# Kernel tuning notes

Measured on AMD Instinct MI355X. Metric: run time of the kernel, lower is better.

## Reference

```python
import jax, jax.numpy as jnp
import numpy as np

B, DIM, X, Y = 2, 256, 48, 48
HEADS, DIM_HEAD = 8, 64
DIM_INNER = HEADS * DIM_HEAD
MASK_SELF_VALUE = -100.0
EPS = 1e-12


def setup_inputs() -> dict:
    key = jax.random.key(0)
    k0, k1, k2, k3, k4 = jax.random.split(key, 5)
    return {
        "fmap": jax.random.normal(k0, (B, DIM, X, Y), dtype=jnp.float32),
        "gamma": jnp.ones((DIM,), dtype=jnp.float32),
        "w_qk": jax.random.normal(k1, (DIM_INNER, DIM), dtype=jnp.float32) * 0.02,
        "w_v": jax.random.normal(k2, (DIM_INNER, DIM), dtype=jnp.float32) * 0.02,
        "null_kv": jax.random.normal(k3, (2, HEADS, DIM_HEAD), dtype=jnp.float32),
        "w_out": jax.random.normal(k4, (DIM, DIM_INNER), dtype=jnp.float32) * 0.02,
    }


def _safe_sqrt(d2):
    # matches torch.cdist subgradient: zero grad at zero distance
    pos = d2 > 0
    return jnp.where(pos, jnp.sqrt(jnp.where(pos, d2, 1.0)), 0.0)


def reference(fmap, gamma, w_qk, w_v, null_kv, w_out):
    b, c, x, y = fmap.shape
    h, dh = HEADS, DIM_HEAD
    n = x * y
    scale = dh ** -0.5

    # ChannelRMSNorm: L2-normalize over channel dim, * sqrt(dim) * gamma
    l2 = jnp.sqrt(jnp.sum(fmap * fmap, axis=1, keepdims=True))
    normed = fmap / jnp.maximum(l2, EPS) * jnp.sqrt(jnp.float32(c)) * gamma[None, :, None, None]

    flat = normed.reshape(b, c, n)                       # b c n
    qk = jnp.einsum('oc,bcn->bon', w_qk, flat)           # b (h d) n
    v = jnp.einsum('oc,bcn->bon', w_v, flat)
    qk = qk.reshape(b, h, dh, n).transpose(0, 1, 3, 2)   # b h n d
    v = v.reshape(b, h, dh, n).transpose(0, 1, 3, 2)

    nk = jnp.broadcast_to(null_kv[0][None, :, None, :], (b, h, 1, dh))
    nv = jnp.broadcast_to(null_kv[1][None, :, None, :], (b, h, 1, dh))
    q = qk
    k = jnp.concatenate([nk, qk], axis=2)                # b h (n+1) d
    vv = jnp.concatenate([nv, v], axis=2)

    # -cdist(q, k, p=2) * scale via squared-distance expansion
    q2 = jnp.sum(q * q, axis=-1)[..., :, None]           # b h n 1
    k2 = jnp.sum(k * k, axis=-1)[..., None, :]           # b h 1 n+1
    cross = jnp.einsum('bhid,bhjd->bhij', q, k)          # b h n n+1
    d2 = jnp.maximum(q2 + k2 - 2.0 * cross, 0.0)
    sim = -_safe_sqrt(d2) * scale

    # mask self: eye(n) left-padded by one (null token never masked)
    self_mask = jnp.eye(n, n + 1, k=1, dtype=bool)
    sim = jnp.where(self_mask, MASK_SELF_VALUE, sim)

    attn = jax.nn.softmax(sim, axis=-1)
    out = jnp.einsum('bhij,bhjd->bhid', attn, vv)        # b h n d
    out = out.transpose(0, 1, 3, 2).reshape(b, h * dh, x, y)
    return jnp.einsum('oc,bcxy->boxy', w_out, out)
```

## Files before the change

kernel.cpp:

```cpp
#include <hip/hip_runtime.h>
#include <math.h>

#define NPOS 2304
#define CC   256
#define DI   512
#define NT   36
#define SCALE 0.125f
#define MASKV -100.0f
#define NEGSL2E (-0.18033688011112042f)

typedef __attribute__((ext_vector_type(8))) short bf16x8;
typedef __attribute__((ext_vector_type(4))) float f32x4;
typedef unsigned short u16;
typedef unsigned int u32;

__device__ inline u16 f2bf(float f) {
    union { float f; unsigned int u; } v; v.f = f;
    return (u16)((v.u + 0x7fffu + ((v.u >> 16) & 1u)) >> 16);
}
__device__ inline float bf2f(u16 h) { return __uint_as_float(((u32)h) << 16); }

__device__ inline bf16x8 ld_x8(const u16* p) {
    union { bf16x8 v; uint2 d[2]; } u;
    u.d[0] = *(const uint2*)(p + 0);
    u.d[1] = *(const uint2*)(p + 4);
    return u.v;
}

__device__ __forceinline__ void gl16(const u16* g, u16* l) {
    __builtin_amdgcn_global_load_lds(
        (const __attribute__((address_space(1))) void*)g,
        (__attribute__((address_space(3))) void*)l, 16, 0, 0);
}

__global__ __launch_bounds__(256) void k_pre(const float* __restrict__ fmap,
                                             const float* __restrict__ gamma,
                                             const float* __restrict__ wqk,
                                             const float* __restrict__ wv,
                                             const float* __restrict__ wout,
                                             u16* __restrict__ xn,
                                             u16* __restrict__ wqkh,
                                             u16* __restrict__ wvh,
                                             u16* __restrict__ wo_hi,
                                             u16* __restrict__ wo_lo) {
    const int blk = blockIdx.x;
    const int t = threadIdx.x;
    if (blk >= 72) {
        const int idx = blk - 72;
        if (idx < 128) {
            const int k = idx * 256 + t;
            const float4 v = ((const float4*)wqk)[k];
            ushort4 h4;
            h4.x = f2bf(v.x); h4.y = f2bf(v.y); h4.z = f2bf(v.z); h4.w = f2bf(v.w);
            ((ushort4*)wqkh)[k] = h4;
        } else if (idx < 256) {
            const int k = (idx - 128) * 256 + t;
            const float4 v = ((const float4*)wv)[k];
            ushort4 h4;
            h4.x = f2bf(v.x); h4.y = f2bf(v.y); h4.z = f2bf(v.z); h4.w = f2bf(v.w);
            ((ushort4*)wvh)[k] = h4;
        } else {
            const int k = (idx - 256) * 256 + t;
            const float4 v = ((const float4*)wout)[k];
            ushort4 h4, l4;
            h4.x = f2bf(v.x); l4.x = f2bf(v.x - bf2f(h4.x));
            h4.y = f2bf(v.y); l4.y = f2bf(v.y - bf2f(h4.y));
            h4.z = f2bf(v.z); l4.z = f2bf(v.z - bf2f(h4.z));
            h4.w = f2bf(v.w); l4.w = f2bf(v.w - bf2f(h4.w));
            ((ushort4*)wo_hi)[k] = h4;
            ((ushort4*)wo_lo)[k] = l4;
        }
        return;
    }
    const int b = blk & 1, n0 = (blk >> 1) * 64;
    const int tx = t & 63, ty = t >> 6;
    __shared__ u16 X[64][260];
    __shared__ float red[4][64];
    __shared__ float inv_s[64];
    __shared__ float gs[256];

    gs[t] = gamma[t];
    const float* fb = fmap + (size_t)b * CC * NPOS;
    float v64[64];
#pragma unroll
    for (int i = 0; i < 64; ++i)
        v64[i] = fb[(ty * 64 + i) * NPOS + n0 + tx];
    float s = 0.0f;
#pragma unroll
    for (int i = 0; i < 64; ++i) s += v64[i] * v64[i];
    red[ty][tx] = s;
    __syncthreads();
    if (t < 64) {
        const float tt = red[0][t] + red[1][t] + red[2][t] + red[3][t];
        inv_s[t] = 16.0f / fmaxf(sqrtf(tt), 1e-12f);
    }
    __syncthreads();
    const float iv = inv_s[tx];
#pragma unroll
    for (int i = 0; i < 64; i += 2) {
        const int c = ty * 64 + i;
        const float v0 = v64[i] * iv * gs[c];
        const float v1 = v64[i + 1] * iv * gs[c + 1];
        *(u32*)&X[tx][c] = (u32)f2bf(v0) | ((u32)f2bf(v1) << 16);
    }
    __syncthreads();
    u16* xb = xn + ((size_t)b * NPOS + n0) * 256;
#pragma unroll
    for (int k = 0; k < 8; ++k) {
        const int gran = k * 256 + t;
        const int row = gran >> 5, colg = gran & 31;
        const uint2 lo = *(const uint2*)&X[row][colg * 8];
        const uint2 hi = *(const uint2*)&X[row][colg * 8 + 4];
        *(uint4*)&xb[(size_t)gran * 8] = make_uint4(lo.x, lo.y, hi.x, hi.y);
    }
}

__global__ __launch_bounds__(256) void k_proj(const u16* __restrict__ xn,
                                              const u16* __restrict__ wqkh,
                                              const u16* __restrict__ wvh,
                                              const float* __restrict__ null_kv,
                                              u16* __restrict__ qkh,
                                              u16* __restrict__ vt,
                                              float* __restrict__ sq,
                                              float* __restrict__ ndot,
                                              float* __restrict__ nk2b) {
    const int blk = blockIdx.x;
    const int xcd = blk & 7;
    const int r   = blk >> 3;
    const int bh  = xcd * 2 + (r & 1);
    const int b   = bh >> 3;
    const int oy  = bh & 7;
    const int n0  = (r >> 1) * 64;

    const int t  = threadIdx.x;
    const int w = t >> 6, lane = t & 63, mcol = lane & 15, quad = lane >> 4;

    __shared__ __align__(16) u16 Xl[16384];
    __shared__ float sqp[4][64], ndp[4][64];
    u16 (*Tt)[68] = (u16(*)[68])Xl;

    const u16* xg = xn + ((size_t)b * NPOS + n0) * 256;
    {
        const int r01 = lane >> 5;
        const int jg = lane & 31;
#pragma unroll
        for (int rr = 0; rr < 8; ++rr) {
            const int row = rr * 8 + w * 2 + r01;
            gl16(xg + (size_t)row * 256 + (size_t)((jg ^ (row & 7)) * 8),
                 Xl + (rr * 8 + w * 2) * 256);
        }
    }
    if (blk == 0 && t < 8) {
        float s2 = 0.0f;
#pragma unroll 8
        for (int d = 0; d < 64; ++d) { const float x = null_kv[t * 64 + d]; s2 += x * x; }
        nk2b[t] = s2;
    }
    __syncthreads();

    const size_t wroff = (size_t)(oy * 64 + w * 16 + mcol) * 256 + quad * 8;
    const u16* wrq = wqkh + wroff;
    const u16* wrv = wvh + wroff;

    f32x4 cq[4], cv[4];
#pragma unroll
    for (int nf = 0; nf < 4; ++nf) {
        cq[nf] = (f32x4){0.f, 0.f, 0.f, 0.f};
        cv[nf] = (f32x4){0.f, 0.f, 0.f, 0.f};
    }
#pragma unroll
    for (int kc = 0; kc < 8; ++kc) {
        const bf16x8 aq = *(const bf16x8*)&wrq[kc * 32];
        const bf16x8 av = *(const bf16x8*)&wrv[kc * 32];
        bf16x8 xB[4];
#pragma unroll
        for (int nf = 0; nf < 4; ++nf) {
            const int row = nf * 16 + mcol;
            const int g = (kc * 4 + quad) ^ (row & 7);
            xB[nf] = *(const bf16x8*)&Xl[row * 256 + g * 8];
        }
#pragma unroll
        for (int nf = 0; nf < 4; ++nf) {
            cq[nf] = __builtin_amdgcn_mfma_f32_16x16x32_bf16(aq, xB[nf], cq[nf], 0, 0, 0);
            cv[nf] = __builtin_amdgcn_mfma_f32_16x16x32_bf16(av, xB[nf], cv[nf], 0, 0, 0);
        }
    }
    __syncthreads();

    {
        const int h = oy;
        const float4 nk4 = *(const float4*)&null_kv[h * 64 + w * 16 + quad * 4];
        float sv[4], nd[4];
#pragma unroll
        for (int nf = 0; nf < 4; ++nf) {
            sv[nf] = cq[nf][0] * cq[nf][0] + cq[nf][1] * cq[nf][1] + cq[nf][2] * cq[nf][2] + cq[nf][3] * cq[nf][3];
            nd[nf] = cq[nf][0] * nk4.x + cq[nf][1] * nk4.y + cq[nf][2] * nk4.z + cq[nf][3] * nk4.w;
        }
#pragma unroll
        for (int mk = 16; mk <= 32; mk <<= 1)
#pragma unroll
            for (int nf = 0; nf < 4; ++nf) {
                sv[nf] += __shfl_xor(sv[nf], mk);
                nd[nf] += __shfl_xor(nd[nf], mk);
            }
        if (quad == 0) {
#pragma unroll
            for (int nf = 0; nf < 4; ++nf) {
                sqp[w][nf * 16 + mcol] = sv[nf];
                ndp[w][nf * 16 + mcol] = nd[nf];
            }
        }
#pragma unroll
        for (int nf = 0; nf < 4; ++nf) {
            ushort4 r4;
            r4.x = f2bf(cq[nf][0]); r4.y = f2bf(cq[nf][1]);
            r4.z = f2bf(cq[nf][2]); r4.w = f2bf(cq[nf][3]);
            *(ushort4*)&Tt[nf * 16 + mcol][w * 16 + quad * 4] = r4;
        }
        __syncthreads();
        {
            const int n = t >> 2, ds = (t & 3) * 16;
            const uint2 r0 = *(const uint2*)&Tt[n][ds + 0];
            const uint2 r1 = *(const uint2*)&Tt[n][ds + 4];
            const uint2 r2 = *(const uint2*)&Tt[n][ds + 8];
            const uint2 r3 = *(const uint2*)&Tt[n][ds + 12];
            u16* dst = qkh + (((size_t)bh) * NPOS + n0 + n) * 64 + ds;
            *(uint4*)&dst[0] = make_uint4(r0.x, r0.y, r1.x, r1.y);
            *(uint4*)&dst[8] = make_uint4(r2.x, r2.y, r3.x, r3.y);
        }
        if (t < 64) {
            sq  [((size_t)bh) * NPOS + n0 + t] = sqp[0][t] + sqp[1][t] + sqp[2][t] + sqp[3][t];
            ndot[((size_t)bh) * NPOS + n0 + t] = ndp[0][t] + ndp[1][t] + ndp[2][t] + ndp[3][t];
        }
    }
    __syncthreads();

    {
#pragma unroll
        for (int nf = 0; nf < 4; ++nf)
#pragma unroll
            for (int rr = 0; rr < 4; ++rr)
                Tt[w * 16 + quad * 4 + rr][nf * 16 + mcol] = f2bf(cv[nf][rr]);
        __syncthreads();
        {
            const int d = t >> 2, ks = t & 3;
            const uint2 a0 = *(const uint2*)&Tt[d][ks * 16 + 0];
            const uint2 a1 = *(const uint2*)&Tt[d][ks * 16 + 4];
            const uint2 a2 = *(const uint2*)&Tt[d][ks * 16 + 8];
            const uint2 a3 = *(const uint2*)&Tt[d][ks * 16 + 12];
            u16* vdst = vt + (size_t)bh * (72 * 64 * 32);
            const int kb = (n0 >> 5) + (ks >> 1);
            u16* p = &vdst[((size_t)kb * 64 + d) * 32 + (ks & 1) * 16];
            *(uint4*)&p[0] = make_uint4(a0.x, a0.y, a1.x, a1.y);
            *(uint4*)&p[8] = make_uint4(a2.x, a2.y, a3.x, a3.y);
        }
    }
}

template <int KS>
__global__ __launch_bounds__(256) void k_attn(const u16* __restrict__ qkh,
                                              const u16* __restrict__ vt,
                                              const float* __restrict__ null_kv,
                                              const float* __restrict__ nk2b,
                                              const float* __restrict__ sq,
                                              const float* __restrict__ ndot,
                                              u16* __restrict__ ih,
                                              u16* __restrict__ il,
                                              float* __restrict__ pO,
                                              float* __restrict__ pL) {
    const int blk = blockIdx.x;
    const int xcd = blk & 7;
    const int j = blk >> 3;
    const int bh = xcd * 2 + (j & 1);
    const int r2 = j >> 1;
    const int qt = (KS == 2) ? (r2 >> 1) : r2;
    const int kh = (KS == 2) ? (r2 & 1) : 0;
    const int q0 = qt * 64;
    const int b = bh >> 3, h = bh & 7;
    const int t = threadIdx.x;
    const int wave = t >> 6, lane = t & 63;
    const int mcol = lane & 15, quad = lane >> 4;

    const int kt0 = kh * 18;
    const int NTL = (KS == 2) ? 18 : 36;

    __shared__ __align__(16) u16 sm[20480];
    u16* Kls = sm;
    u16* Vls = sm + 8192;
    u16 (*Pt)[64] = (u16(*)[64])(sm + 16384 + wave * 1024);

    const u16* qbase = qkh + (size_t)bh * NPOS * 64;
    const u16* vbase = vt + (size_t)bh * (72 * 64 * 32);
    const float* sqb = sq + (size_t)bh * NPOS;

    const int q16 = q0 + wave * 16;
    const bf16x8 bq00 = *(const bf16x8*)&qbase[(q16 + mcol) * 64 + quad * 8];
    const bf16x8 bq01 = *(const bf16x8*)&qbase[(q16 + mcol) * 64 + 32 + quad * 8];
    const float q2 = sqb[q16 + mcol];
    const int ktm = q16 >> 6;
    const int nbm = (q16 >> 4) & 3;

    const int kbase0 = (wave * 16 + 0) * 64;
    const int kbase1 = (wave * 16 + 8) * 64;
    const int ksrc0 = (wave * 16 + 0 + (lane >> 3)) * 64 + ((lane & 7) ^ (lane >> 3)) * 8;
    const int ksrc1 = (wave * 16 + 8 + (lane >> 3)) * 64 + ((lane & 7) ^ (lane >> 3)) * 8;
    const int vldsb = wave * 512;
    const int vsrc = (wave * 16 + (lane >> 2)) * 32 + ((lane & 3) ^ ((lane >> 3) & 3)) * 8;

    const int m7 = mcol & 7;
    const int mv = (mcol >> 1) & 3;

    {
        const u16* kg = qbase + (size_t)kt0 * 4096;
        const u16* vg = vbase + (size_t)kt0 * 4096;
        gl16(kg + ksrc0, Kls + kbase0);
        gl16(kg + ksrc1, Kls + kbase1);
        gl16(vg + vsrc,        Vls + vldsb);
        gl16(vg + 2048 + vsrc, Vls + 2048 + vldsb);
    }

    const bf16x8 ones = {0x3F80, 0x3F80, 0x3F80, 0x3F80, 0x3F80, 0x3F80, 0x3F80, 0x3F80};

    f32x4 oacc[4];
#pragma unroll
    for (int nb = 0; nb < 4; ++nb) oacc[nb] = (f32x4){0.f, 0.f, 0.f, 0.f};
    f32x4 lsum = (f32x4){0.f, 0.f, 0.f, 0.f};

    int p = 0;
#pragma unroll 1
    for (int i = 0; i < NTL; ++i) {
        const int kt = kt0 + i;
        __syncthreads();
        float4 k2q[4];
#pragma unroll
        for (int nb = 0; nb < 4; ++nb)
            k2q[nb] = *(const float4*)&sqb[kt * 64 + nb * 16 + quad * 4];
        if (i + 1 < NTL) {
            const u16* kg = qbase + (size_t)(kt + 1) * 4096;
            const u16* vg = vbase + (size_t)(kt + 1) * 4096;
            const int bb = (p ^ 1) * 4096;
            gl16(kg + ksrc0, Kls + bb + kbase0);
            gl16(kg + ksrc1, Kls + bb + kbase1);
            gl16(vg + vsrc,        Vls + bb + vldsb);
            gl16(vg + 2048 + vsrc, Vls + bb + 2048 + vldsb);
        }

        const u16* Kb = Kls + p * 4096;
        const u16* Vb = Vls + p * 4096;

        bf16x8 bk[4][2];
#pragma unroll
        for (int nb = 0; nb < 4; ++nb) {
            const int rr = (nb * 16 + mcol) * 64;
            bk[nb][0] = *(const bf16x8*)&Kb[rr + ((quad ^ m7)) * 8];
            bk[nb][1] = *(const bf16x8*)&Kb[rr + (((4 + quad) ^ m7)) * 8];
        }

        f32x4 c[4];
#pragma unroll
        for (int nb = 0; nb < 4; ++nb) {
            c[nb] = (f32x4){0.f, 0.f, 0.f, 0.f};
            c[nb] = __builtin_amdgcn_mfma_f32_16x16x32_bf16(bk[nb][0], bq00, c[nb], 0, 0, 0);
            c[nb] = __builtin_amdgcn_mfma_f32_16x16x32_bf16(bk[nb][1], bq01, c[nb], 0, 0, 0);
        }

        bf16x8 bv[4][2];
#pragma unroll
        for (int nb = 0; nb < 4; ++nb) {
            const int rr = (nb * 16 + mcol) * 32 + ((quad ^ mv)) * 8;
            bv[nb][0] = *(const bf16x8*)&Vb[rr];
            bv[nb][1] = *(const bf16x8*)&Vb[2048 + rr];
        }

#pragma unroll
        for (int nb = 0; nb < 4; ++nb) {
            float e[4];
#pragma unroll
            for (int r = 0; r < 4; ++r) {
                const float pre = q2 + ((const float*)&k2q[nb])[r];
                const float d2 = fmaxf(__builtin_fmaf(c[nb][r], -2.0f, pre), 0.0f);
                e[r] = __builtin_amdgcn_exp2f(NEGSL2E * __builtin_amdgcn_sqrtf(d2));
            }
            if (kt == ktm && nb == nbm) {
#pragma unroll
                for (int r = 0; r < 4; ++r)
                    if (quad * 4 + r == mcol) e[r] = 0.0f;
            }
            const u32 p01 = __builtin_amdgcn_perm(__float_as_uint(e[1]), __float_as_uint(e[0]), 0x07060302u);
            const u32 p23 = __builtin_amdgcn_perm(__float_as_uint(e[3]), __float_as_uint(e[2]), 0x07060302u);
            *(uint2*)&Pt[mcol][(((nb * 4 + quad) ^ (m7 << 1))) * 4] = make_uint2(p01, p23);
        }

        const bf16x8 bp00 = *(const bf16x8*)&Pt[mcol][(quad ^ m7) * 8];
        const bf16x8 bp01 = *(const bf16x8*)&Pt[mcol][((4 + quad) ^ m7) * 8];

#pragma unroll
        for (int nb = 0; nb < 4; ++nb) {
            oacc[nb] = __builtin_amdgcn_mfma_f32_16x16x32_bf16(bv[nb][0], bp00, oacc[nb], 0, 0, 0);
            oacc[nb] = __builtin_amdgcn_mfma_f32_16x16x32_bf16(bv[nb][1], bp01, oacc[nb], 0, 0, 0);
        }
        lsum = __builtin_amdgcn_mfma_f32_16x16x32_bf16(ones, bp00, lsum, 0, 0, 0);
        lsum = __builtin_amdgcn_mfma_f32_16x16x32_bf16(ones, bp01, lsum, 0, 0, 0);

        p ^= 1;
    }

    __syncthreads();

    float* Ofin = (float*)sm + wave * (16 * 68);
#pragma unroll
    for (int nb = 0; nb < 4; ++nb)
        *(f32x4*)&Ofin[mcol * 68 + nb * 16 + quad * 4] = oacc[nb];
    if (quad == 0) Ofin[mcol * 68 + 64] = lsum[0];

    {
        const int q = lane >> 2;
        const int d0 = (lane & 3) * 16;
        const float4 a0 = *(const float4*)&Ofin[q * 68 + d0 + 0];
        const float4 a1 = *(const float4*)&Ofin[q * 68 + d0 + 4];
        const float4 a2 = *(const float4*)&Ofin[q * 68 + d0 + 8];
        const float4 a3 = *(const float4*)&Ofin[q * 68 + d0 + 12];
        const float l = Ofin[q * 68 + 64];
        const int qg = q16 + q;

        if (KS == 2) {
            float* dst = pO + (size_t)kh * 2359296 + ((size_t)bh * NPOS + qg) * 64 + d0;
            *(float4*)&dst[0]  = a0;
            *(float4*)&dst[4]  = a1;
            *(float4*)&dst[8]  = a2;
            *(float4*)&dst[12] = a3;
            if ((lane & 3) == 0)
                pL[(size_t)kh * 36864 + (size_t)bh * NPOS + qg] = l;
        } else {
            const float q2v = sqb[qg];
            const float nd = ndot[(size_t)bh * NPOS + qg];
            const float nk2 = nk2b[h];
            const float d2n = fmaxf(q2v + nk2 - 2.0f * nd, 0.0f);
            const float beta = __expf(-sqrtf(d2n) * SCALE);
            const float ilv = 1.0f / (l + beta);

            const float* nvp = &null_kv[DI + h * 64 + d0];
            const float4 nv0 = *(const float4*)&nvp[0];
            const float4 nv1 = *(const float4*)&nvp[4];
            const float4 nv2 = *(const float4*)&nvp[8];
            const float4 nv3 = *(const float4*)&nvp[12];

            const size_t ob = ((size_t)b * NPOS + qg) * DI + h * 64 + d0;
            float vv[16];
            vv[0]  = (a0.x + beta * nv0.x) * ilv; vv[1]  = (a0.y + beta * nv0.y) * ilv;
            vv[2]  = (a0.z + beta * nv0.z) * ilv; vv[3]  = (a0.w + beta * nv0.w) * ilv;
            vv[4]  = (a1.x + beta * nv1.x) * ilv; vv[5]  = (a1.y + beta * nv1.y) * ilv;
            vv[6]  = (a1.z + beta * nv1.z) * ilv; vv[7]  = (a1.w + beta * nv1.w) * ilv;
            vv[8]  = (a2.x + beta * nv2.x) * ilv; vv[9]  = (a2.y + beta * nv2.y) * ilv;
            vv[10] = (a2.z + beta * nv2.z) * ilv; vv[11] = (a2.w + beta * nv2.w) * ilv;
            vv[12] = (a3.x + beta * nv3.x) * ilv; vv[13] = (a3.y + beta * nv3.y) * ilv;
            vv[14] = (a3.z + beta * nv3.z) * ilv; vv[15] = (a3.w + beta * nv3.w) * ilv;
#pragma unroll
            for (int g = 0; g < 4; ++g) {
                ushort4 hi4, lo4;
                hi4.x = f2bf(vv[g * 4 + 0]); lo4.x = f2bf(vv[g * 4 + 0] - bf2f(hi4.x));
                hi4.y = f2bf(vv[g * 4 + 1]); lo4.y = f2bf(vv[g * 4 + 1] - bf2f(hi4.y));
                hi4.z = f2bf(vv[g * 4 + 2]); lo4.z = f2bf(vv[g * 4 + 2] - bf2f(hi4.z));
                hi4.w = f2bf(vv[g * 4 + 3]); lo4.w = f2bf(vv[g * 4 + 3] - bf2f(hi4.w));
                *(ushort4*)&ih[ob + g * 4] = hi4;
                *(ushort4*)&il[ob + g * 4] = lo4;
            }
        }
    }
}

__global__ __launch_bounds__(256) void k_merge(const float* __restrict__ pO,
                                               const float* __restrict__ pL,
                                               const float* __restrict__ null_kv,
                                               const float* __restrict__ nk2b,
                                               const float* __restrict__ sq,
                                               const float* __restrict__ ndot,
                                               u16* __restrict__ ih,
                                               u16* __restrict__ il) {
    const int gid = blockIdx.x * 256 + (int)threadIdx.x;
    const int d0 = (gid & 3) * 16;
    const int t2 = gid >> 2;
    const int bh = t2 / NPOS;
    const int qg = t2 - bh * NPOS;
    const int b = bh >> 3, h = bh & 7;

    const size_t o0 = ((size_t)bh * NPOS + qg) * 64 + d0;
    const size_t o1 = o0 + 2359296;
    const float4 a0 = *(const float4*)&pO[o0 + 0];
    const float4 a1 = *(const float4*)&pO[o0 + 4];
    const float4 a2 = *(const float4*)&pO[o0 + 8];
    const float4 a3 = *(const float4*)&pO[o0 + 12];
    const float4 c0 = *(const float4*)&pO[o1 + 0];
    const float4 c1 = *(const float4*)&pO[o1 + 4];
    const float4 c2 = *(const float4*)&pO[o1 + 8];
    const float4 c3 = *(const float4*)&pO[o1 + 12];
    const float l = pL[(size_t)bh * NPOS + qg] + pL[36864 + (size_t)bh * NPOS + qg];

    const float q2v = sq[(size_t)bh * NPOS + qg];
    const float nd = ndot[(size_t)bh * NPOS + qg];
    const float nk2 = nk2b[h];
    const float d2n = fmaxf(q2v + nk2 - 2.0f * nd, 0.0f);
    const float beta = __expf(-sqrtf(d2n) * SCALE);
    const float ilv = 1.0f / (l + beta);

    const float* nvp = &null_kv[DI + h * 64 + d0];
    const float4 nv0 = *(const float4*)&nvp[0];
    const float4 nv1 = *(const float4*)&nvp[4];
    const float4 nv2 = *(const float4*)&nvp[8];
    const float4 nv3 = *(const float4*)&nvp[12];

    float vv[16];
    vv[0]  = (a0.x + c0.x + beta * nv0.x) * ilv; vv[1]  = (a0.y + c0.y + beta * nv0.y) * ilv;
    vv[2]  = (a0.z + c0.z + beta * nv0.z) * ilv; vv[3]  = (a0.w + c0.w + beta * nv0.w) * ilv;
    vv[4]  = (a1.x + c1.x + beta * nv1.x) * ilv; vv[5]  = (a1.y + c1.y + beta * nv1.y) * ilv;
    vv[6]  = (a1.z + c1.z + beta * nv1.z) * ilv; vv[7]  = (a1.w + c1.w + beta * nv1.w) * ilv;
    vv[8]  = (a2.x + c2.x + beta * nv2.x) * ilv; vv[9]  = (a2.y + c2.y + beta * nv2.y) * ilv;
    vv[10] = (a2.z + c2.z + beta * nv2.z) * ilv; vv[11] = (a2.w + c2.w + beta * nv2.w) * ilv;
    vv[12] = (a3.x + c3.x + beta * nv3.x) * ilv; vv[13] = (a3.y + c3.y + beta * nv3.y) * ilv;
    vv[14] = (a3.z + c3.z + beta * nv3.z) * ilv; vv[15] = (a3.w + c3.w + beta * nv3.w) * ilv;

    const size_t ob = ((size_t)b * NPOS + qg) * DI + h * 64 + d0;
#pragma unroll
    for (int g = 0; g < 4; ++g) {
        ushort4 hi4, lo4;
        hi4.x = f2bf(vv[g * 4 + 0]); lo4.x = f2bf(vv[g * 4 + 0] - bf2f(hi4.x));
        hi4.y = f2bf(vv[g * 4 + 1]); lo4.y = f2bf(vv[g * 4 + 1] - bf2f(hi4.y));
        hi4.z = f2bf(vv[g * 4 + 2]); lo4.z = f2bf(vv[g * 4 + 2] - bf2f(hi4.z));
        hi4.w = f2bf(vv[g * 4 + 3]); lo4.w = f2bf(vv[g * 4 + 3] - bf2f(hi4.w));
        *(ushort4*)&ih[ob + g * 4] = hi4;
        *(ushort4*)&il[ob + g * 4] = lo4;
    }
}

__global__ __launch_bounds__(256) void k_out(const u16* __restrict__ wo_hi,
                                             const u16* __restrict__ wo_lo,
                                             const u16* __restrict__ ih,
                                             const u16* __restrict__ il,
                                             float* __restrict__ out) {
    const int j0 = blockIdx.x * 32;
    const int c0 = blockIdx.y * 64;
    const int b  = blockIdx.z;
    const int t  = threadIdx.x;
    const int w = t >> 6, lane = t & 63, mcol = lane & 15, quad = lane >> 4;

    __shared__ __align__(16) u16 Bst[2][2][32][64];

    const u16* ah = wo_hi + (size_t)(c0 + w * 16 + mcol) * 512 + quad * 8;
    const u16* al = wo_lo + (size_t)(c0 + w * 16 + mcol) * 512 + quad * 8;

    const size_t bsrc_row = (size_t)b * NPOS + j0 + w * 8 + (lane >> 3);
    const int bsg = ((lane & 7) ^ (lane >> 3)) * 8;
    const u16* bsrc_h = ih + bsrc_row * 512 + bsg;
    const u16* bsrc_l = il + bsrc_row * 512 + bsg;
    u16* bdst_h = &Bst[0][0][w * 8][0];
    u16* bdst_l = &Bst[0][1][w * 8][0];

    gl16(bsrc_h, bdst_h);
    gl16(bsrc_l, bdst_l);

    f32x4 c[2];
    c[0] = (f32x4){0.f, 0.f, 0.f, 0.f};
    c[1] = (f32x4){0.f, 0.f, 0.f, 0.f};

    int p = 0;
#pragma unroll 1
    for (int ph = 0; ph < 8; ++ph) {
        __syncthreads();
        if (ph + 1 < 8) {
            const int ko = (ph + 1) * 64;
            gl16(bsrc_h + ko, bdst_h + (p ^ 1) * 4096);
            gl16(bsrc_l + ko, bdst_l + (p ^ 1) * 4096);
        }
        const u16* Bb = &Bst[p][0][0][0];
#pragma unroll
        for (int sub = 0; sub < 2; ++sub) {
            const int kc = ph * 2 + sub;
            const bf16x8 A  = *(const bf16x8*)&ah[kc * 32];
            const bf16x8 Al = *(const bf16x8*)&al[kc * 32];
#pragma unroll
            for (int nf = 0; nf < 2; ++nf) {
                const int r = nf * 16 + mcol;
                const int g = (sub * 4 + quad) ^ (r & 7);
                const bf16x8 Bh = *(const bf16x8*)&Bb[r * 64 + g * 8];
                const bf16x8 Bl = *(const bf16x8*)&Bb[2048 + r * 64 + g * 8];
                c[nf] = __builtin_amdgcn_mfma_f32_16x16x32_bf16(A,  Bh, c[nf], 0, 0, 0);
                c[nf] = __builtin_amdgcn_mfma_f32_16x16x32_bf16(A,  Bl, c[nf], 0, 0, 0);
                c[nf] = __builtin_amdgcn_mfma_f32_16x16x32_bf16(Al, Bh, c[nf], 0, 0, 0);
            }
        }
        p ^= 1;
    }
    float* ob = out + ((size_t)b * CC + c0 + w * 16) * NPOS + j0;
#pragma unroll
    for (int nf = 0; nf < 2; ++nf)
#pragma unroll
        for (int r = 0; r < 4; ++r)
            ob[(size_t)(quad * 4 + r) * NPOS + nf * 16 + mcol] = c[nf][r];
}

extern "C" void kernel_launch(void* const* d_in, const int* in_sizes, int n_in,
                              void* d_out, int out_size, void* d_ws, size_t ws_size,
                              hipStream_t stream) {
    const float* fmap    = (const float*)d_in[0];
    const float* gamma   = (const float*)d_in[1];
    const float* w_qk    = (const float*)d_in[2];
    const float* w_v     = (const float*)d_in[3];
    const float* null_kv = (const float*)d_in[4];
    const float* w_out   = (const float*)d_in[5];
    float* out = (float*)d_out;

    u16* ws16 = (u16*)d_ws;
    u16* qkh    = ws16;
    u16* vtb    = qkh + 2359296;
    u16* in_hi  = vtb + 2359296;
    u16* in_lo  = in_hi + 2359296;
    u16* wo_hi  = in_lo + 2359296;
    u16* wo_lo  = wo_hi + 131072;
    u16* wqkh   = wo_lo + 131072;
    u16* wvh    = wqkh + 131072;
    u16* xnb    = wvh + 131072;
    float* sqbuf = (float*)(xnb + 1179648);
    float* ndbuf = sqbuf + 36864;
    float* nk2b  = ndbuf + 36864;
    float* pOws  = nk2b + 8;
    float* pLws  = pOws + 4718592;
    const size_t need_split = (size_t)((char*)(pLws + 73728) - (char*)d_ws);

    hipLaunchKernelGGL(k_pre,  dim3(456),       dim3(256), 0, stream,
                       fmap, gamma, w_qk, w_v, w_out, xnb, wqkh, wvh, wo_hi, wo_lo);
    hipLaunchKernelGGL(k_proj, dim3(576),       dim3(256), 0, stream,
                       xnb, wqkh, wvh, null_kv, qkh, vtb, sqbuf, ndbuf, nk2b);
    if (ws_size >= need_split) {
        hipLaunchKernelGGL(HIP_KERNEL_NAME(k_attn<2>), dim3(1152), dim3(256), 0, stream,
                           qkh, vtb, null_kv, nk2b, sqbuf, ndbuf, in_hi, in_lo, pOws, pLws);
        hipLaunchKernelGGL(k_merge, dim3(576),  dim3(256), 0, stream,
                           pOws, pLws, null_kv, nk2b, sqbuf, ndbuf, in_hi, in_lo);
    } else {
        hipLaunchKernelGGL(HIP_KERNEL_NAME(k_attn<1>), dim3(576), dim3(256), 0, stream,
                           qkh, vtb, null_kv, nk2b, sqbuf, ndbuf, in_hi, in_lo, pOws, pLws);
    }
    hipLaunchKernelGGL(k_out,  dim3(72, 4, 2),  dim3(256), 0, stream,
                       wo_hi, wo_lo, in_hi, in_lo, out);
}
```

Before: 157.4 us.

## Fuse split-K merge into attention via atomic counters; split QK/V projection blocks

Removes the separate k_merge launch. Each attention split now increments a per-tile atomic counter, and whichever split arrives second merges the partial outputs and writes the bf16 hi/lo results. Counters are zeroed in k_pre. The projection kernel now launches twice as many blocks, each computing either QK or V, which raises parallelism but loads the X tile twice. The cost is extra fences, an atomic per tile and a serialized merge tail in the last-arriving block.

```diff
diff --git a/kernel.cpp b/kernel.cpp
--- a/kernel.cpp
+++ b/kernel.cpp
@@ -42,11 +42,15 @@
                                              u16* __restrict__ wqkh,
                                              u16* __restrict__ wvh,
                                              u16* __restrict__ wo_hi,
-                                             u16* __restrict__ wo_lo) {
+                                             u16* __restrict__ wo_lo,
+                                             int* __restrict__ mflags) {
     const int blk = blockIdx.x;
     const int t = threadIdx.x;
     if (blk >= 72) {
         const int idx = blk - 72;
+        if (idx == 0 && mflags) {
+            for (int i = t; i < 576; i += 256) mflags[i] = 0;
+        }
         if (idx < 128) {
             const int k = idx * 256 + t;
             const float4 v = ((const float4*)wqk)[k];
@@ -124,7 +128,9 @@
                                               float* __restrict__ sq,
                                               float* __restrict__ ndot,
                                               float* __restrict__ nk2b) {
-    const int blk = blockIdx.x;
+    const int blk0 = blockIdx.x;
+    const int isv = blk0 >= 576;
+    const int blk = isv ? blk0 - 576 : blk0;
     const int xcd = blk & 7;
     const int r   = blk >> 3;
     const int bh  = xcd * 2 + (r & 1);
@@ -150,7 +156,7 @@
                  Xl + (rr * 8 + w * 2) * 256);
         }
     }
-    if (blk == 0 && t < 8) {
+    if (blk0 == 0 && t < 8) {
         float s2 = 0.0f;
 #pragma unroll 8
         for (int d = 0; d < 64; ++d) { const float x = null_kv[t * 64 + d]; s2 += x * x; }
@@ -159,19 +165,14 @@
     __syncthreads();
 
     const size_t wroff = (size_t)(oy * 64 + w * 16 + mcol) * 256 + quad * 8;
-    const u16* wrq = wqkh + wroff;
-    const u16* wrv = wvh + wroff;
-
-    f32x4 cq[4], cv[4];
-#pragma unroll
-    for (int nf = 0; nf < 4; ++nf) {
-        cq[nf] = (f32x4){0.f, 0.f, 0.f, 0.f};
-        cv[nf] = (f32x4){0.f, 0.f, 0.f, 0.f};
-    }
+    const u16* wr = (isv ? wvh : wqkh) + wroff;
+
+    f32x4 cc[4];
+#pragma unroll
+    for (int nf = 0; nf < 4; ++nf) cc[nf] = (f32x4){0.f, 0.f, 0.f, 0.f};
 #pragma unroll
     for (int kc = 0; kc < 8; ++kc) {
-        const bf16x8 aq = *(const bf16x8*)&wrq[kc * 32];
-        const bf16x8 av = *(const bf16x8*)&wrv[kc * 32];
+        const bf16x8 aw = *(const bf16x8*)&wr[kc * 32];
         bf16x8 xB[4];
 #pragma unroll
         for (int nf = 0; nf < 4; ++nf) {
@@ -180,21 +181,19 @@
             xB[nf] = *(const bf16x8*)&Xl[row * 256 + g * 8];
         }
 #pragma unroll
-        for (int nf = 0; nf < 4; ++nf) {
-            cq[nf] = __builtin_amdgcn_mfma_f32_16x16x32_bf16(aq, xB[nf], cq[nf], 0, 0, 0);
-            cv[nf] = __builtin_amdgcn_mfma_f32_16x16x32_bf16(av, xB[nf], cv[nf], 0, 0, 0);
-        }
+        for (int nf = 0; nf < 4; ++nf)
+            cc[nf] = __builtin_amdgcn_mfma_f32_16x16x32_bf16(aw, xB[nf], cc[nf], 0, 0, 0);
     }
     __syncthreads();
 
-    {
+    if (!isv) {
         const int h = oy;
         const float4 nk4 = *(const float4*)&null_kv[h * 64 + w * 16 + quad * 4];
         float sv[4], nd[4];
 #pragma unroll
         for (int nf = 0; nf < 4; ++nf) {
-            sv[nf] = cq[nf][0] * cq[nf][0] + cq[nf][1] * cq[nf][1] + cq[nf][2] * cq[nf][2] + cq[nf][3] * cq[nf][3];
-            nd[nf] = cq[nf][0] * nk4.x + cq[nf][1] * nk4.y + cq[nf][2] * nk4.z + cq[nf][3] * nk4.w;
+            sv[nf] = cc[nf][0] * cc[nf][0] + cc[nf][1] * cc[nf][1] + cc[nf][2] * cc[nf][2] + cc[nf][3] * cc[nf][3];
+            nd[nf] = cc[nf][0] * nk4.x + cc[nf][1] * nk4.y + cc[nf][2] * nk4.z + cc[nf][3] * nk4.w;
         }
 #pragma unroll
         for (int mk = 16; mk <= 32; mk <<= 1)
@@ -213,8 +212,8 @@
 #pragma unroll
         for (int nf = 0; nf < 4; ++nf) {
             ushort4 r4;
-            r4.x = f2bf(cq[nf][0]); r4.y = f2bf(cq[nf][1]);
-            r4.z = f2bf(cq[nf][2]); r4.w = f2bf(cq[nf][3]);
+            r4.x = f2bf(cc[nf][0]); r4.y = f2bf(cc[nf][1]);
+            r4.z = f2bf(cc[nf][2]); r4.w = f2bf(cc[nf][3]);
             *(ushort4*)&Tt[nf * 16 + mcol][w * 16 + quad * 4] = r4;
         }
         __syncthreads();
@@ -232,15 +231,12 @@
             sq  [((size_t)bh) * NPOS + n0 + t] = sqp[0][t] + sqp[1][t] + sqp[2][t] + sqp[3][t];
             ndot[((size_t)bh) * NPOS + n0 + t] = ndp[0][t] + ndp[1][t] + ndp[2][t] + ndp[3][t];
         }
-    }
-    __syncthreads();
-
-    {
+    } else {
 #pragma unroll
         for (int nf = 0; nf < 4; ++nf)
 #pragma unroll
             for (int rr = 0; rr < 4; ++rr)
-                Tt[w * 16 + quad * 4 + rr][nf * 16 + mcol] = f2bf(cv[nf][rr]);
+                Tt[w * 16 + quad * 4 + rr][nf * 16 + mcol] = f2bf(cc[nf][rr]);
         __syncthreads();
         {
             const int d = t >> 2, ks = t & 3;
@@ -267,7 +263,8 @@
                                               u16* __restrict__ ih,
                                               u16* __restrict__ il,
                                               float* __restrict__ pO,
-                                              float* __restrict__ pL) {
+                                              float* __restrict__ pL,
+                                              int* __restrict__ mflags) {
     const int blk = blockIdx.x;
     const int xcd = blk & 7;
     const int j = blk >> 3;
@@ -467,68 +464,66 @@
             }
         }
     }
-}
-
-__global__ __launch_bounds__(256) void k_merge(const float* __restrict__ pO,
-                                               const float* __restrict__ pL,
-                                               const float* __restrict__ null_kv,
-                                               const float* __restrict__ nk2b,
-                                               const float* __restrict__ sq,
-                                               const float* __restrict__ ndot,
-                                               u16* __restrict__ ih,
-                                               u16* __restrict__ il) {
-    const int gid = blockIdx.x * 256 + (int)threadIdx.x;
-    const int d0 = (gid & 3) * 16;
-    const int t2 = gid >> 2;
-    const int bh = t2 / NPOS;
-    const int qg = t2 - bh * NPOS;
-    const int b = bh >> 3, h = bh & 7;
-
-    const size_t o0 = ((size_t)bh * NPOS + qg) * 64 + d0;
-    const size_t o1 = o0 + 2359296;
-    const float4 a0 = *(const float4*)&pO[o0 + 0];
-    const float4 a1 = *(const float4*)&pO[o0 + 4];
-    const float4 a2 = *(const float4*)&pO[o0 + 8];
-    const float4 a3 = *(const float4*)&pO[o0 + 12];
-    const float4 c0 = *(const float4*)&pO[o1 + 0];
-    const float4 c1 = *(const float4*)&pO[o1 + 4];
-    const float4 c2 = *(const float4*)&pO[o1 + 8];
-    const float4 c3 = *(const float4*)&pO[o1 + 12];
-    const float l = pL[(size_t)bh * NPOS + qg] + pL[36864 + (size_t)bh * NPOS + qg];
-
-    const float q2v = sq[(size_t)bh * NPOS + qg];
-    const float nd = ndot[(size_t)bh * NPOS + qg];
-    const float nk2 = nk2b[h];
-    const float d2n = fmaxf(q2v + nk2 - 2.0f * nd, 0.0f);
-    const float beta = __expf(-sqrtf(d2n) * SCALE);
-    const float ilv = 1.0f / (l + beta);
-
-    const float* nvp = &null_kv[DI + h * 64 + d0];
-    const float4 nv0 = *(const float4*)&nvp[0];
-    const float4 nv1 = *(const float4*)&nvp[4];
-    const float4 nv2 = *(const float4*)&nvp[8];
-    const float4 nv3 = *(const float4*)&nvp[12];
-
-    float vv[16];
-    vv[0]  = (a0.x + c0.x + beta * nv0.x) * ilv; vv[1]  = (a0.y + c0.y + beta * nv0.y) * ilv;
-    vv[2]  = (a0.z + c0.z + beta * nv0.z) * ilv; vv[3]  = (a0.w + c0.w + beta * nv0.w) * ilv;
-    vv[4]  = (a1.x + c1.x + beta * nv1.x) * ilv; vv[5]  = (a1.y + c1.y + beta * nv1.y) * ilv;
-    vv[6]  = (a1.z + c1.z + beta * nv1.z) * ilv; vv[7]  = (a1.w + c1.w + beta * nv1.w) * ilv;
-    vv[8]  = (a2.x + c2.x + beta * nv2.x) * ilv; vv[9]  = (a2.y + c2.y + beta * nv2.y) * ilv;
-    vv[10] = (a2.z + c2.z + beta * nv2.z) * ilv; vv[11] = (a2.w + c2.w + beta * nv2.w) * ilv;
-    vv[12] = (a3.x + c3.x + beta * nv3.x) * ilv; vv[13] = (a3.y + c3.y + beta * nv3.y) * ilv;
-    vv[14] = (a3.z + c3.z + beta * nv3.z) * ilv; vv[15] = (a3.w + c3.w + beta * nv3.w) * ilv;
-
-    const size_t ob = ((size_t)b * NPOS + qg) * DI + h * 64 + d0;
-#pragma unroll
-    for (int g = 0; g < 4; ++g) {
-        ushort4 hi4, lo4;
-        hi4.x = f2bf(vv[g * 4 + 0]); lo4.x = f2bf(vv[g * 4 + 0] - bf2f(hi4.x));
-        hi4.y = f2bf(vv[g * 4 + 1]); lo4.y = f2bf(vv[g * 4 + 1] - bf2f(hi4.y));
-        hi4.z = f2bf(vv[g * 4 + 2]); lo4.z = f2bf(vv[g * 4 + 2] - bf2f(hi4.z));
-        hi4.w = f2bf(vv[g * 4 + 3]); lo4.w = f2bf(vv[g * 4 + 3] - bf2f(hi4.w));
-        *(ushort4*)&ih[ob + g * 4] = hi4;
-        *(ushort4*)&il[ob + g * 4] = lo4;
+
+    if (KS == 2) {
+        __threadfence();
+        __syncthreads();
+        if (t == 0)
+            ((volatile int*)sm)[0] = atomicAdd(&mflags[bh * 36 + qt], 1);
+        __syncthreads();
+        const int old = ((volatile int*)sm)[0];
+        if (old == 1) {
+            __threadfence();
+            const int qg = q0 + (t >> 2);
+            const int d0 = (t & 3) * 16;
+
+            const size_t o0 = ((size_t)bh * NPOS + qg) * 64 + d0;
+            const size_t o1 = o0 + 2359296;
+            const float4 a0 = *(const float4*)&pO[o0 + 0];
+            const float4 a1 = *(const float4*)&pO[o0 + 4];
+            const float4 a2 = *(const float4*)&pO[o0 + 8];
+            const float4 a3 = *(const float4*)&pO[o0 + 12];
+            const float4 c0 = *(const float4*)&pO[o1 + 0];
+            const float4 c1 = *(const float4*)&pO[o1 + 4];
+            const float4 c2 = *(const float4*)&pO[o1 + 8];
+            const float4 c3 = *(const float4*)&pO[o1 + 12];
+            const float l = pL[(size_t)bh * NPOS + qg] + pL[36864 + (size_t)bh * NPOS + qg];
+
+            const float q2v = sqb[qg];
+            const float nd = ndot[(size_t)bh * NPOS + qg];
+            const float nk2 = nk2b[h];
+            const float d2n = fmaxf(q2v + nk2 - 2.0f * nd, 0.0f);
+            const float beta = __expf(-sqrtf(d2n) * SCALE);
+            const float ilv = 1.0f / (l + beta);
+
+            const float* nvp = &null_kv[DI + h * 64 + d0];
+            const float4 nv0 = *(const float4*)&nvp[0];
+            const float4 nv1 = *(const float4*)&nvp[4];
+            const float4 nv2 = *(const float4*)&nvp[8];
+            const float4 nv3 = *(const float4*)&nvp[12];
+
+            float vv[16];
+            vv[0]  = (a0.x + c0.x + beta * nv0.x) * ilv; vv[1]  = (a0.y + c0.y + beta * nv0.y) * ilv;
+            vv[2]  = (a0.z + c0.z + beta * nv0.z) * ilv; vv[3]  = (a0.w + c0.w + beta * nv0.w) * ilv;
+            vv[4]  = (a1.x + c1.x + beta * nv1.x) * ilv; vv[5]  = (a1.y + c1.y + beta * nv1.y) * ilv;
+            vv[6]  = (a1.z + c1.z + beta * nv1.z) * ilv; vv[7]  = (a1.w + c1.w + beta * nv1.w) * ilv;
+            vv[8]  = (a2.x + c2.x + beta * nv2.x) * ilv; vv[9]  = (a2.y + c2.y + beta * nv2.y) * ilv;
+            vv[10] = (a2.z + c2.z + beta * nv2.z) * ilv; vv[11] = (a2.w + c2.w + beta * nv2.w) * ilv;
+            vv[12] = (a3.x + c3.x + beta * nv3.x) * ilv; vv[13] = (a3.y + c3.y + beta * nv3.y) * ilv;
+            vv[14] = (a3.z + c3.z + beta * nv3.z) * ilv; vv[15] = (a3.w + c3.w + beta * nv3.w) * ilv;
+
+            const size_t ob = ((size_t)b * NPOS + qg) * DI + h * 64 + d0;
+#pragma unroll
+            for (int g = 0; g < 4; ++g) {
+                ushort4 hi4, lo4;
+                hi4.x = f2bf(vv[g * 4 + 0]); lo4.x = f2bf(vv[g * 4 + 0] - bf2f(hi4.x));
+                hi4.y = f2bf(vv[g * 4 + 1]); lo4.y = f2bf(vv[g * 4 + 1] - bf2f(hi4.y));
+                hi4.z = f2bf(vv[g * 4 + 2]); lo4.z = f2bf(vv[g * 4 + 2] - bf2f(hi4.z));
+                hi4.w = f2bf(vv[g * 4 + 3]); lo4.w = f2bf(vv[g * 4 + 3] - bf2f(hi4.w));
+                *(ushort4*)&ih[ob + g * 4] = hi4;
+                *(ushort4*)&il[ob + g * 4] = lo4;
+            }
+        }
     }
 }
 
@@ -624,20 +619,21 @@
     float* nk2b  = ndbuf + 36864;
     float* pOws  = nk2b + 8;
     float* pLws  = pOws + 4718592;
-    const size_t need_split = (size_t)((char*)(pLws + 73728) - (char*)d_ws);
+    int*   mflg  = (int*)(pLws + 73728);
+    const size_t need_split = (size_t)((char*)(mflg + 576) - (char*)d_ws);
+    const bool split = (ws_size >= need_split);
 
     hipLaunchKernelGGL(k_pre,  dim3(456),       dim3(256), 0, stream,
-                       fmap, gamma, w_qk, w_v, w_out, xnb, wqkh, wvh, wo_hi, wo_lo);
-    hipLaunchKernelGGL(k_proj, dim3(576),       dim3(256), 0, stream,
+                       fmap, gamma, w_qk, w_v, w_out, xnb, wqkh, wvh, wo_hi, wo_lo,
+                       split ? mflg : (int*)nullptr);
+    hipLaunchKernelGGL(k_proj, dim3(1152),      dim3(256), 0, stream,
                        xnb, wqkh, wvh, null_kv, qkh, vtb, sqbuf, ndbuf, nk2b);
-    if (ws_size >= need_split) {
+    if (split) {
         hipLaunchKernelGGL(HIP_KERNEL_NAME(k_attn<2>), dim3(1152), dim3(256), 0, stream,
-                           qkh, vtb, null_kv, nk2b, sqbuf, ndbuf, in_hi, in_lo, pOws, pLws);
-        hipLaunchKernelGGL(k_merge, dim3(576),  dim3(256), 0, stream,
-                           pOws, pLws, null_kv, nk2b, sqbuf, ndbuf, in_hi, in_lo);
+                           qkh, vtb, null_kv, nk2b, sqbuf, ndbuf, in_hi, in_lo, pOws, pLws, mflg);
     } else {
         hipLaunchKernelGGL(HIP_KERNEL_NAME(k_attn<1>), dim3(576), dim3(256), 0, stream,
-                           qkh, vtb, null_kv, nk2b, sqbuf, ndbuf, in_hi, in_lo, pOws, pLws);
+                           qkh, vtb, null_kv, nk2b, sqbuf, ndbuf, in_hi, in_lo, pOws, pLws, mflg);
     }
     hipLaunchKernelGGL(k_out,  dim3(72, 4, 2),  dim3(256), 0, stream,
                        wo_hi, wo_lo, in_hi, in_lo, out);
```

Result: slower. 369.0 us (+134.5%).
